# Kernel optimization log

Hardware: AMD Instinct MI355X
Metric: run time of the kernel (lower is better)

## Reference

```python
import jax, jax.numpy as jnp
import numpy as np

DIM = 1024; SD = 1024; N_BANDS = 4; MIMO_P = 8; BATCH = 2; L = 2048
LOG10000 = float(np.log(10000.0))


def _hippo_freqs(sd):
    n = jnp.arange(sd, dtype=jnp.float32)
    f = jnp.sqrt(2.0 * n + 1.0)
    f = f / f[-1]
    return jnp.exp(-f * LOG10000)


def setup_inputs() -> dict:
    key = jax.random.key(0)
    ks = jax.random.split(key, 16)
    dim, sd = DIM, SD
    wscale = 1.0 / np.sqrt(dim)
    n = jnp.arange(sd, dtype=jnp.float32)
    b0 = jnp.sqrt(2.0 * n + 1.0); b0 = b0 / b0[-1]
    b0_inv = jnp.log(jnp.expm1(jnp.clip(b0, 1e-6, None)))  # softplus^-1 of hippo b
    G = sd // MIMO_P
    inp = dict(
        x=jax.random.normal(ks[0], (BATCH, L, dim), jnp.float32),
        z_prev=jax.random.normal(ks[1], (BATCH, L, dim), jnp.float32),
        W_psi=jax.random.normal(ks[2], (2 * sd, dim), jnp.float32) * wscale,
        b_psi=jnp.zeros(2 * sd, jnp.float32),
        W_phi=jax.random.normal(ks[3], (2 * sd, dim), jnp.float32) * wscale,
        b_phi=jnp.zeros(2 * sd, jnp.float32),
        W_gate=jax.random.normal(ks[4], (1, dim), jnp.float32) * wscale,
        b_gate=jnp.zeros(1, jnp.float32),
        surprise_gain=jnp.zeros(1, jnp.float32),
        omega=_hippo_freqs(sd),
        log_gamma=jax.random.normal(ks[5], (sd,), jnp.float32) * 0.5 - 7.0,
        dt=jnp.float32(np.log(np.expm1(0.1))),  # layer_idx=0, depth=1 -> target_dt=0.1
        W_bs=jax.random.normal(ks[6], (sd, dim), jnp.float32) * 0.02,
        b_bs=b0_inv,
        W_ps=jax.random.uniform(ks[7], (sd, dim), jnp.float32, -wscale, wscale),
        b_ps=jnp.zeros(sd, jnp.float32),
        W_btx=jax.random.normal(ks[8], (sd, dim), jnp.float32) * 0.02,
        b_btx=b0_inv,
        W_bth=jax.random.normal(ks[9], (sd, 2 * sd), jnp.float32) * 0.02,
        b_bth=jnp.zeros(sd, jnp.float32),
        W_ptx=jax.random.uniform(ks[10], (sd, dim), jnp.float32, -wscale, wscale),
        b_ptx=jnp.zeros(sd, jnp.float32),
        mimo_w=jnp.eye(MIMO_P, dtype=jnp.float32)[None].repeat(G, 0)
               + 0.02 * jax.random.normal(ks[11], (G, MIMO_P, MIMO_P), jnp.float32),
        tau=jnp.ones(1, jnp.float32),
        beta=jnp.zeros(1, jnp.float32),
    )
    return inp


def _forward(x, z_prev, W_psi, b_psi, W_phi, b_phi, W_gate, b_gate, surprise_gain,
             omega, log_gamma, dt, W_bs, b_bs, W_ps, b_ps, W_btx, b_btx,
             W_bth, b_bth, W_ptx, b_ptx, mimo_w, tau, beta):
    Bsz, Ls, D = x.shape
    sd = omega.shape[0]
    n_fft = 1 << (2 * Ls - 1).bit_length()  # static

    # unitary mask: band 0 = lowest hippo frequencies (slowest modes) stay lossless
    freqs = _hippo_freqs(sd)
    order = jnp.argsort(freqs)
    band0 = order[: sd // N_BANDS]
    not_unitary = jnp.ones(sd, jnp.float32).at[band0].set(0.0)

    lin = lambda a, W, bb: a @ W.T + bb

    psi_raw = lin(x, W_psi, b_psi)
    psi = jax.lax.complex(psi_raw[..., :sd], psi_raw[..., sd:])
    phi_raw = lin(x, W_phi, b_phi)
    phi = jax.lax.complex(phi_raw[..., :sd], phi_raw[..., sd:])

    gate = jax.nn.sigmoid(lin(x, W_gate, b_gate))  # [B,L,1]
    surprise = jnp.mean(jnp.abs(x - z_prev), -1, keepdims=True)
    gate = gate * (1.0 + jnp.tanh(surprise_gain) * surprise)

    dt_eff = jax.nn.softplus(dt)
    gamma_eff = jax.nn.softplus(log_gamma) * not_unitary
    lam = jax.lax.complex(-gamma_eff, omega)  # [SD]
    t = jnp.arange(Ls, dtype=jnp.float32)
    kernel_raw = jnp.exp(lam[None, :] * (t[:, None] * dt_eff))  # [L,SD] A^t
    k_pad = jnp.concatenate([jnp.zeros((2, sd), kernel_raw.dtype), kernel_raw], 0)
    kernel_simpson = (k_pad[2:] + 4.0 * k_pad[1:-1] + k_pad[:-2]) / 6.0  # Simpson taps

    Kf_scout = jnp.fft.fft(kernel_raw.T, n=n_fft, axis=1)      # [SD,n_fft]
    Kf_true = jnp.fft.fft(kernel_simpson.T, n=n_fft, axis=1)

    def fftconv(U, Kf):  # causal conv via FFT: U [B,L,SD] complex
        Uf = jnp.fft.fft(jnp.transpose(U, (0, 2, 1)), n=n_fft, axis=2)
        H = jnp.fft.ifft(Uf * Kf[None], axis=2)[:, :, :Ls]
        return jnp.transpose(H, (0, 2, 1))

    # ---- scout wave: input-only LTI ----
    b_scout = jax.nn.softplus(lin(x, W_bs, b_bs))
    ph_s = jnp.pi * jnp.tanh(lin(x, W_ps, b_ps))
    Bc_s = jax.lax.complex(b_scout * jnp.cos(ph_s), b_scout * jnp.sin(ph_s))
    U_scout = gate * Bc_s * psi
    H_scout = fftconv(U_scout, Kf_scout)
    H_prev = jnp.pad(H_scout, ((0, 0), (1, 0), (0, 0)))[:, :-1]  # shift by 1
    scout_rms = jnp.sqrt(jnp.mean(H_prev.real ** 2 + H_prev.imag ** 2, -1, keepdims=True) + 1e-6)
    Hn = H_prev / scout_rms
    H_flat = jnp.concatenate([Hn.real, Hn.imag], -1)  # [B,L,2SD]

    # ---- true wave: state-dependent B, Simpson quadrature kernel ----
    b_true = jax.nn.softplus(lin(x, W_btx, b_btx) + lin(H_flat, W_bth, b_bth))
    ph_t = jnp.pi * jnp.tanh(lin(x, W_ptx, b_ptx))
    Bc_t = jax.lax.complex(b_true * jnp.cos(ph_t), b_true * jnp.sin(ph_t))
    U_true = gate * Bc_t * psi
    H = fftconv(U_true, Kf_true)

    read_rms = jnp.sqrt(jnp.mean(H.real ** 2 + H.imag ** 2, -1, keepdims=True) + 1e-6)
    Hn2 = H / read_rms

    # block-diagonal MIMO mixing in groups of mimo_p
    G = sd // MIMO_P
    Hg = Hn2.reshape(Bsz, Ls, G, MIMO_P)
    Hm = jnp.einsum('blgp,gpq->blgq', Hg, mimo_w.astype(Hg.dtype)).reshape(Bsz, Ls, sd)

    # Born-rule measurement: out = Re(h * phi^*), affine read temperature
    out = jnp.real(Hm * jnp.conj(phi))
    return tau * out + beta  # SD == dim -> out_proj is Identity


def reference(x, z_prev, W_psi, b_psi, W_phi, b_phi, W_gate, b_gate, surprise_gain,
              omega, log_gamma, dt, W_bs, b_bs, W_ps, b_ps, W_btx, b_btx,
              W_bth, b_bth, W_ptx, b_ptx, mimo_w, tau, beta):
    return _forward(x, z_prev, W_psi, b_psi, W_phi, b_phi, W_gate, b_gate,
                    surprise_gain, omega, log_gamma, dt, W_bs, b_bs, W_ps, b_ps,
                    W_btx, b_btx, W_bth, b_bth, W_ptx, b_ptx, mimo_w, tau, beta)
```

## Files before the change

kernel.cpp:

```cpp
#include <hip/hip_runtime.h>
#include <math.h>

#define DIMX   1024
#define SDN    1024
#define BATCHN 2
#define LSEQ   2048
#define BLROWS (BATCHN*LSEQ)
#define NCHUNK 64
#define LCHUNK (LSEQ/NCHUNK)
#define PI_F   3.14159265358979f

typedef unsigned short ushort_t;
typedef unsigned int uint_t;
typedef __bf16 bf16_t;
typedef bf16_t bf16x8 __attribute__((ext_vector_type(8)));
typedef float f32x4 __attribute__((ext_vector_type(4)));

__device__ __forceinline__ float softplusf_(float x) {
  return x > 20.0f ? x : log1pf(expf(x));
}

__device__ __forceinline__ ushort_t f2bf_rne(float f) {
  unsigned u = __float_as_uint(f);
  u = u + 0x7fffu + ((u >> 16) & 1u);
  return (ushort_t)(u >> 16);
}

__device__ __forceinline__ float bf2f(ushort_t u) {
  return __uint_as_float(((unsigned)u) << 16);
}

__device__ __forceinline__ uint_t pk2(float2 v) {
  return (uint_t)f2bf_rne(v.x) | ((uint_t)f2bf_rne(v.y) << 16);
}
__device__ __forceinline__ float2 upk2(uint_t u) {
  return make_float2(__uint_as_float(u << 16), __uint_as_float(u & 0xffff0000u));
}

__device__ __forceinline__ float2 cfma2(float2 a, float2 v, float2 u) {
  float re = fmaf(a.x, v.x, fmaf(-a.y, v.y, u.x));
  float im = fmaf(a.x, v.y, fmaf(a.y, v.x, u.y));
  return make_float2(re, im);
}

__device__ __forceinline__ void gload_lds16(const ushort_t* g, ushort_t* l) {
  __builtin_amdgcn_global_load_lds(
      (const __attribute__((address_space(1))) void*)g,
      (__attribute__((address_space(3))) void*)l, 16, 0, 0);
}

__global__ __launch_bounds__(256) void wcvt_kernel(
    const float* __restrict__ x,
    const float* __restrict__ Wpsi, const float* __restrict__ Wphi,
    const float* __restrict__ Wbs, const float* __restrict__ Wps,
    const float* __restrict__ Wbtx, const float* __restrict__ Wptx,
    const float* __restrict__ Wbth,
    const float* __restrict__ b_psi, const float* __restrict__ b_phi,
    const float* __restrict__ b_bs, const float* __restrict__ b_ps,
    const float* __restrict__ b_btx, const float* __restrict__ b_ptx,
    ushort_t* __restrict__ xb, ushort_t* __restrict__ wcat,
    ushort_t* __restrict__ wbthb, float* __restrict__ bcat) {
  int b = blockIdx.x;
  if (b >= 14336) {
    int n = (b - 14336) * 256 + threadIdx.x;
    float v;
    if (n < 2048) v = b_psi[n];
    else if (n < 4096) v = b_phi[n - 2048];
    else if (n < 5120) v = b_bs[n - 4096];
    else if (n < 6144) v = b_ps[n - 5120];
    else if (n < 7168) v = b_btx[n - 6144];
    else v = b_ptx[n - 7168];
    bcat[n] = v;
    return;
  }
  const float* src; ushort_t* dst; int off;
  if (b < 4096)       { src = x;    dst = xb;               off = b; }
  else if (b < 6144)  { src = Wpsi; dst = wcat;             off = b - 4096; }
  else if (b < 8192)  { src = Wphi; dst = wcat + 2097152u;  off = b - 6144; }
  else if (b < 9216)  { src = Wbs;  dst = wcat + 4194304u;  off = b - 8192; }
  else if (b < 10240) { src = Wps;  dst = wcat + 5242880u;  off = b - 9216; }
  else if (b < 11264) { src = Wbtx; dst = wcat + 6291456u;  off = b - 10240; }
  else if (b < 12288) { src = Wptx; dst = wcat + 7340032u;  off = b - 11264; }
  else                { src = Wbth; dst = wbthb;            off = b - 12288; }
  int i = (off * 256 + threadIdx.x) * 4;
  float4 v = *(const float4*)(src + i);
  ushort4 o;
  o.x = f2bf_rne(v.x); o.y = f2bf_rne(v.y);
  o.z = f2bf_rne(v.z); o.w = f2bf_rne(v.w);
  *(ushort4*)(dst + i) = o;
}

__global__ void coef_kernel(const float* __restrict__ omega,
                            const float* __restrict__ log_gamma,
                            const float* __restrict__ dt,
                            float2* __restrict__ a_out,
                            float2* __restrict__ A_out) {
  int s = blockIdx.x * blockDim.x + threadIdx.x;
  if (s >= SDN) return;
  double dtv = (double)dt[0];
  double dte = dtv > 20.0 ? dtv : log1p(exp(dtv));
  double gam = 0.0;
  if (s < SDN - SDN / 4) {
    double lg = (double)log_gamma[s];
    gam = lg > 20.0 ? lg : log1p(exp(lg));
  }
  double th = (double)omega[s] * dte;
  double r  = exp(-gam * dte);
  a_out[s] = make_float2((float)(r * cos(th)), (float)(r * sin(th)));
  double thl = th * (double)LCHUNK;
  double rl  = exp(-gam * dte * (double)LCHUNK);
  A_out[s] = make_float2((float)(rl * cos(thl)), (float)(rl * sin(thl)));
}

__global__ __launch_bounds__(256) void gate_kernel(
    const float* __restrict__ x, const float* __restrict__ z,
    const float* __restrict__ Wg, const float* __restrict__ bg,
    const float* __restrict__ sg, float* __restrict__ gate) {
  int m = blockIdx.x * 4 + (threadIdx.x >> 6);
  int lane = threadIdx.x & 63;
  const float* xp = x + (size_t)m * DIMX;
  const float* zp = z + (size_t)m * DIMX;
  float dot = 0.f, sur = 0.f;
  for (int i = lane; i < DIMX; i += 64) {
    float xv = xp[i];
    dot = fmaf(xv, Wg[i], dot);
    sur += fabsf(xv - zp[i]);
  }
#pragma unroll
  for (int o = 32; o > 0; o >>= 1) {
    dot += __shfl_down(dot, o, 64);
    sur += __shfl_down(sur, o, 64);
  }
  if (lane == 0) {
    float gs = 1.f / (1.f + expf(-(dot + bg[0])));
    gate[m] = gs * (1.f + tanhf(sg[0]) * (sur * (1.f / DIMX)));
  }
}

template<int MODE>
__global__ __launch_bounds__(256, 2) void gemm_bf16(
    const ushort_t* __restrict__ Xb, const ushort_t* __restrict__ Wb,
    const float* __restrict__ bias, ushort_t* __restrict__ Cb) {
  __shared__ ushort_t As[2][4096];
  __shared__ ushort_t Bs[2][4096];
  const int tid = threadIdx.x;
  const int w = tid >> 6, l = tid & 63;
  int bm, bn, ldx, ldw;
  const ushort_t *Xp, *Wp;
  if (MODE == 0) {
    int b = blockIdx.x;
    int xcd = b & 7, idx = b >> 3;
    int tx = ((xcd & 3) << 4) + (idx & 15);
    int ty = ((xcd >> 2) << 4) + (idx >> 4);
    bm = ty << 7; bn = tx << 7;
    ldx = 1024; ldw = 1024;
    Xp = Xb; Wp = Wb;
  } else {
    bm = blockIdx.y << 7; bn = blockIdx.x << 7;
    ldx = 2048; ldw = 2048;
    Xp = Xb + blockIdx.z * 1024;
    Wp = Wb + blockIdx.z * 1024;
  }
  const int wr = w >> 1, wc = w & 1;

  const int srow = tid >> 2;
  const int c8 = (((tid & 3) - (tid >> 3)) & 3) << 3;
  const ushort_t* ga0 = Xp + (size_t)(bm + srow) * ldx + c8;
  const ushort_t* ga1 = Xp + (size_t)(bm + 64 + srow) * ldx + c8;
  const ushort_t* gb0 = Wp + (size_t)(bn + srow) * ldw + c8;
  const ushort_t* gb1 = Wp + (size_t)(bn + 64 + srow) * ldw + c8;

  f32x4 acc[4][4] = {};
  const int nk = 32;

#define STAGE(buf, kt)                                   \
  do {                                                   \
    gload_lds16(ga0 + (kt), &As[buf][w * 512]);          \
    gload_lds16(ga1 + (kt), &As[buf][2048 + w * 512]);   \
    gload_lds16(gb0 + (kt), &Bs[buf][w * 512]);          \
    gload_lds16(gb1 + (kt), &Bs[buf][2048 + w * 512]);   \
  } while (0)

  STAGE(0, 0);
  __syncthreads();

  const int rl = l & 15, kh = l >> 4;
  const int chunkp = (kh + (rl >> 1)) & 3;
  for (int kt = 0; kt < nk; ++kt) {
    int cur = kt & 1;
    if (kt + 1 < nk) STAGE(cur ^ 1, (kt + 1) * 32);
    const uint4* Af = (const uint4*)As[cur];
    const uint4* Bf = (const uint4*)Bs[cur];
    bf16x8 a[4], b[4];
#pragma unroll
    for (int i = 0; i < 4; ++i)
      a[i] = __builtin_bit_cast(bf16x8, Af[(wr * 64 + i * 16 + rl) * 4 + chunkp]);
#pragma unroll
    for (int j = 0; j < 4; ++j)
      b[j] = __builtin_bit_cast(bf16x8, Bf[(wc * 64 + j * 16 + rl) * 4 + chunkp]);
#pragma unroll
    for (int i = 0; i < 4; ++i)
#pragma unroll
      for (int j = 0; j < 4; ++j)
        acc[i][j] = __builtin_amdgcn_mfma_f32_16x16x32_bf16(a[i], b[j], acc[i][j], 0, 0, 0);
    __syncthreads();
  }
#undef STAGE

#pragma unroll
  for (int i = 0; i < 4; ++i) {
    int mrow = bm + wr * 64 + i * 16 + (l >> 4) * 4;
#pragma unroll
    for (int j = 0; j < 4; ++j) {
      int ncol = bn + wc * 64 + j * 16 + (l & 15);
      if (MODE == 0) {
        float bv = bias[ncol];
#pragma unroll
        for (int r = 0; r < 4; ++r)
          Cb[(size_t)(mrow + r) * 8192 + ncol] = f2bf_rne(acc[i][j][r] + bv);
      } else {
        ushort_t* P = Cb + (size_t)blockIdx.z * (4096u * 1024u);
#pragma unroll
        for (int r = 0; r < 4; ++r)
          P[(size_t)(mrow + r) * 1024 + ncol] = f2bf_rne(acc[i][j][r]);
      }
    }
  }
}


__global__ __launch_bounds__(256) void u_scout(
    const float* __restrict__ gate, const ushort_t* __restrict__ proj,
    uint_t* __restrict__ U) {
  int idx = blockIdx.x * 256 + threadIdx.x;
  int m = idx >> 10, s = idx & (SDN - 1);
  const ushort_t* pr = proj + ((size_t)m << 13);
  float g  = gate[m];
  float bv = softplusf_(bf2f(pr[4096 + s]));
  float ph = PI_F * tanhf(bf2f(pr[5120 + s]));
  float sph, cph;
  sincosf(ph, &sph, &cph);
  float br = bv * cph, bi = bv * sph;
  float pre = bf2f(pr[s]), pim = bf2f(pr[1024 + s]);
  U[idx] = pk2(make_float2(g * (br * pre - bi * pim), g * (br * pim + bi * pre)));
}

__global__ __launch_bounds__(256) void u_true(
    const float* __restrict__ gate, const ushort_t* __restrict__ proj,
    const ushort_t* __restrict__ P0, const ushort_t* __restrict__ P1,
    const float* __restrict__ b_bth, uint_t* __restrict__ U) {
  int idx = blockIdx.x * 256 + threadIdx.x;
  int m = idx >> 10, s = idx & (SDN - 1);
  const ushort_t* pr = proj + ((size_t)m << 13);
  float g  = gate[m];
  float blv = bf2f(pr[6144 + s]) + bf2f(P0[idx]) + bf2f(P1[idx]) + b_bth[s];
  float bv = softplusf_(blv);
  float ph = PI_F * tanhf(bf2f(pr[7168 + s]));
  float sph, cph;
  sincosf(ph, &sph, &cph);
  float br = bv * cph, bi = bv * sph;
  float pre = bf2f(pr[s]), pim = bf2f(pr[1024 + s]);
  U[idx] = pk2(make_float2(g * (br * pre - bi * pim), g * (br * pim + bi * pre)));
}

__global__ __launch_bounds__(256) void scan_stage1(
    const uint_t* __restrict__ U, const float2* __restrict__ a,
    float2* __restrict__ carry) {
  int s = blockIdx.x * 256 + threadIdx.x;
  int c = blockIdx.y, b = blockIdx.z;
  float2 av = a[s];
  float2 V = make_float2(0.f, 0.f);
  const uint_t* Up = U + (size_t)(b * LSEQ + c * LCHUNK) * SDN + s;
#pragma unroll 4
  for (int t = 0; t < LCHUNK; ++t)
    V = cfma2(av, V, upk2(Up[(size_t)t * SDN]));
  carry[(size_t)(b * NCHUNK + c) * SDN + s] = V;
}

__global__ __launch_bounds__(256) void scan_stage2(
    const float2* __restrict__ carry, const float2* __restrict__ A,
    float2* __restrict__ prefix) {
  int s = blockIdx.x * 256 + threadIdx.x;
  int b = blockIdx.z;
  float2 Av = A[s];
  float2 P = make_float2(0.f, 0.f);
  for (int c = 0; c < NCHUNK; ++c) {
    size_t off = (size_t)(b * NCHUNK + c) * SDN + s;
    prefix[off] = P;
    P = cfma2(Av, P, carry[off]);
  }
}

__global__ __launch_bounds__(256) void scan_stage3(
    const uint_t* __restrict__ U, const float2* __restrict__ a,
    const float2* __restrict__ prefix, uint_t* __restrict__ Vout) {
  int s = blockIdx.x * 256 + threadIdx.x;
  int c = blockIdx.y, b = blockIdx.z;
  float2 av = a[s];
  float2 V = prefix[(size_t)(b * NCHUNK + c) * SDN + s];
  size_t base = (size_t)(b * LSEQ + c * LCHUNK) * SDN + s;
#pragma unroll 4
  for (int t = 0; t < LCHUNK; ++t) {
    V = cfma2(av, V, upk2(U[base + (size_t)t * SDN]));
    Vout[base + (size_t)t * SDN] = pk2(V);
  }
}

__global__ __launch_bounds__(256) void hflat_kernel(
    const uint_t* __restrict__ V, ushort_t* __restrict__ Hflat) {
  int m = blockIdx.x;
  int t = m & (LSEQ - 1);
  float2 v[4];
  float sum = 0.f;
#pragma unroll
  for (int i = 0; i < 4; ++i) {
    int s = threadIdx.x + i * 256;
    float2 vv = make_float2(0.f, 0.f);
    if (t > 0) vv = upk2(V[(size_t)(m - 1) * SDN + s]);
    v[i] = vv;
    sum += vv.x * vv.x + vv.y * vv.y;
  }
  __shared__ float red[256];
  red[threadIdx.x] = sum;
  __syncthreads();
  for (int o = 128; o > 0; o >>= 1) {
    if (threadIdx.x < o) red[threadIdx.x] += red[threadIdx.x + o];
    __syncthreads();
  }
  float inv = 1.0f / sqrtf(red[0] * (1.f / SDN) + 1e-6f);
  ushort_t* hr = Hflat + ((size_t)m << 11);
#pragma unroll
  for (int i = 0; i < 4; ++i) {
    int s = threadIdx.x + i * 256;
    hr[s] = f2bf_rne(v[i].x * inv);
    hr[SDN + s] = f2bf_rne(v[i].y * inv);
  }
}

__global__ __launch_bounds__(256) void final_kernel(
    const uint_t* __restrict__ V, const ushort_t* __restrict__ proj,
    const float* __restrict__ mimo, const float* __restrict__ tau,
    const float* __restrict__ beta, float* __restrict__ out) {
  int bid = blockIdx.x;
  int m = ((bid & 7) << 9) | (bid >> 3);
  int t = m & (LSEQ - 1);
  __shared__ float2 hl[SDN];
  __shared__ float red[256];
  float sum = 0.f;
#pragma unroll
  for (int i = 0; i < 4; ++i) {
    int s = threadIdx.x + i * 256;
    float2 v0 = upk2(V[(size_t)m * SDN + s]);
    float2 v1 = make_float2(0.f, 0.f), v2 = make_float2(0.f, 0.f);
    if (t >= 1) v1 = upk2(V[(size_t)(m - 1) * SDN + s]);
    if (t >= 2) v2 = upk2(V[(size_t)(m - 2) * SDN + s]);
    float2 h = make_float2((v0.x + 4.f * v1.x + v2.x) * (1.f / 6.f),
                           (v0.y + 4.f * v1.y + v2.y) * (1.f / 6.f));
    hl[s] = h;
    sum += h.x * h.x + h.y * h.y;
  }
  red[threadIdx.x] = sum;
  __syncthreads();
  for (int o = 128; o > 0; o >>= 1) {
    if (threadIdx.x < o) red[threadIdx.x] += red[threadIdx.x + o];
    __syncthreads();
  }
  float inv = 1.0f / sqrtf(red[0] * (1.f / SDN) + 1e-6f);
  float tv = tau[0], bv = beta[0];
  const ushort_t* pp = proj + ((size_t)m << 13) + 2048;
#pragma unroll
  for (int i = 0; i < 4; ++i) {
    int s = threadIdx.x + i * 256;
    int g = s >> 3, q = s & 7;
    const float* wp = mimo + (size_t)g * 64 + q;
    float hr = 0.f, hi = 0.f;
#pragma unroll
    for (int p = 0; p < 8; ++p) {
      float wv = wp[p * 8];
      float2 hp = hl[(g << 3) + p];
      hr = fmaf(hp.x, wv, hr);
      hi = fmaf(hp.y, wv, hi);
    }
    hr *= inv; hi *= inv;
    float o1 = hr * bf2f(pp[s]) + hi * bf2f(pp[SDN + s]);
    out[(size_t)m * SDN + s] = tv * o1 + bv;
  }
}

extern "C" void kernel_launch(void* const* d_in, const int* in_sizes, int n_in,
                              void* d_out, int out_size, void* d_ws, size_t ws_size,
                              hipStream_t stream) {
  const float* x      = (const float*)d_in[0];
  const float* z_prev = (const float*)d_in[1];
  const float* W_psi  = (const float*)d_in[2];
  const float* b_psi  = (const float*)d_in[3];
  const float* W_phi  = (const float*)d_in[4];
  const float* b_phi  = (const float*)d_in[5];
  const float* W_gate = (const float*)d_in[6];
  const float* b_gate = (const float*)d_in[7];
  const float* s_gain = (const float*)d_in[8];
  const float* omega  = (const float*)d_in[9];
  const float* log_g  = (const float*)d_in[10];
  const float* dt     = (const float*)d_in[11];
  const float* W_bs   = (const float*)d_in[12];
  const float* b_bs   = (const float*)d_in[13];
  const float* W_ps   = (const float*)d_in[14];
  const float* b_ps   = (const float*)d_in[15];
  const float* W_btx  = (const float*)d_in[16];
  const float* b_btx  = (const float*)d_in[17];
  const float* W_bth  = (const float*)d_in[18];
  const float* b_bth  = (const float*)d_in[19];
  const float* W_ptx  = (const float*)d_in[20];
  const float* b_ptx  = (const float*)d_in[21];
  const float* mimo_w = (const float*)d_in[22];
  const float* tau    = (const float*)d_in[23];
  const float* beta   = (const float*)d_in[24];
  float* out = (float*)d_out;

  float* ws = (float*)d_ws;
  const size_t M1 = 1 << 20;
  ushort_t* proj   = (ushort_t*)ws;
  uint_t*   U      = (uint_t*)(ws + 16 * M1);
  uint_t*   V      = U;
  ushort_t* xb     = (ushort_t*)(ws + 24 * M1);
  ushort_t* wcat   = (ushort_t*)(ws + 26 * M1);
  ushort_t* P0     = wcat;
  ushort_t* P1     = wcat + 4u * 1024u * 1024u;
  ushort_t* wbthb  = (ushort_t*)(ws + 30 * M1);
  ushort_t* hflatB = (ushort_t*)(ws + 31 * M1);
  float*    bcat   = ws + 35 * M1;
  float*    gate   = bcat + 8192;
  float2*   ac     = (float2*)(gate + 4096);
  float2*   Ac     = ac + 1024;
  float2*   carry  = Ac + 1024;
  float2*   prefix = carry + 131072;
  (void)ws_size; (void)in_sizes; (void)n_in; (void)out_size;

  dim3 blk(256);
  dim3 sgrid(SDN / 256, NCHUNK, BATCHN);

  coef_kernel<<<dim3(4), blk, 0, stream>>>(omega, log_g, dt, ac, Ac);
  gate_kernel<<<dim3(BLROWS / 4), blk, 0, stream>>>(x, z_prev, W_gate, b_gate, s_gain, gate);
  wcvt_kernel<<<dim3(14368), blk, 0, stream>>>(
      x, W_psi, W_phi, W_bs, W_ps, W_btx, W_ptx, W_bth,
      b_psi, b_phi, b_bs, b_ps, b_btx, b_ptx,
      xb, wcat, wbthb, bcat);

  gemm_bf16<0><<<dim3(2048), blk, 0, stream>>>(xb, wcat, bcat, proj);

  u_scout<<<dim3(BLROWS * SDN / 256), blk, 0, stream>>>(gate, proj, U);
  scan_stage1<<<sgrid, blk, 0, stream>>>(U, ac, carry);
  scan_stage2<<<dim3(SDN / 256, 1, BATCHN), blk, 0, stream>>>(carry, Ac, prefix);
  scan_stage3<<<sgrid, blk, 0, stream>>>(U, ac, prefix, V);

  hflat_kernel<<<dim3(BLROWS), blk, 0, stream>>>(V, hflatB);
  gemm_bf16<1><<<dim3(8, 32, 2), blk, 0, stream>>>(hflatB, wbthb, bcat, P0);

  u_true<<<dim3(BLROWS * SDN / 256), blk, 0, stream>>>(gate, proj, P0, P1, b_bth, U);
  scan_stage1<<<sgrid, blk, 0, stream>>>(U, ac, carry);
  scan_stage2<<<dim3(SDN / 256, 1, BATCHN), blk, 0, stream>>>(carry, Ac, prefix);
  scan_stage3<<<sgrid, blk, 0, stream>>>(U, ac, prefix, V);

  final_kernel<<<dim3(BLROWS), blk, 0, stream>>>(V, proj, mimo_w, tau, beta, out);
}
```

Baseline: 239.2 us.

## Fuse prep kernels, vectorize U builders with fast math, unroll scans more

Merges the coefficient, gate and weight-conversion kernels into one prep kernel, and computes the gate from the same x loads used for the bf16 conversion. The u_scout and u_true kernels now handle two elements per thread with packed 32-bit loads and stores. They also use fast intrinsics (__expf/__logf softplus, an exp-based tanh, __sincosf) in place of precise libm calls. Scan loops get deeper unrolling. The goal is to cut launch overhead and redundant reads of x, and to make the elementwise kernels cheaper, at the cost of some accuracy in the transcendental functions.

```diff
diff --git a/kernel.cpp b/kernel.cpp
--- a/kernel.cpp
+++ b/kernel.cpp
@@ -16,10 +16,6 @@
 typedef bf16_t bf16x8 __attribute__((ext_vector_type(8)));
 typedef float f32x4 __attribute__((ext_vector_type(4)));
 
-__device__ __forceinline__ float softplusf_(float x) {
-  return x > 20.0f ? x : log1pf(expf(x));
-}
-
 __device__ __forceinline__ ushort_t f2bf_rne(float f) {
   unsigned u = __float_as_uint(f);
   u = u + 0x7fffu + ((u >> 16) & 1u);
@@ -43,14 +39,23 @@
   return make_float2(re, im);
 }
 
+__device__ __forceinline__ float fast_softplus(float x) {
+  return x > 15.f ? x : __logf(1.f + __expf(x));
+}
+__device__ __forceinline__ float fast_tanh(float x) {
+  float xc = fminf(fmaxf(x, -9.f), 9.f);
+  float t = __expf(2.f * xc);
+  return (t - 1.f) * __builtin_amdgcn_rcpf(t + 1.f);
+}
+
 __device__ __forceinline__ void gload_lds16(const ushort_t* g, ushort_t* l) {
   __builtin_amdgcn_global_load_lds(
       (const __attribute__((address_space(1))) void*)g,
       (__attribute__((address_space(3))) void*)l, 16, 0, 0);
 }
 
-__global__ __launch_bounds__(256) void wcvt_kernel(
-    const float* __restrict__ x,
+__global__ __launch_bounds__(256) void prep_kernel(
+    const float* __restrict__ x, const float* __restrict__ z_prev,
     const float* __restrict__ Wpsi, const float* __restrict__ Wphi,
     const float* __restrict__ Wbs, const float* __restrict__ Wps,
     const float* __restrict__ Wbtx, const float* __restrict__ Wptx,
@@ -58,11 +63,64 @@
     const float* __restrict__ b_psi, const float* __restrict__ b_phi,
     const float* __restrict__ b_bs, const float* __restrict__ b_ps,
     const float* __restrict__ b_btx, const float* __restrict__ b_ptx,
+    const float* __restrict__ Wg, const float* __restrict__ bg,
+    const float* __restrict__ sg,
+    const float* __restrict__ omega, const float* __restrict__ log_gamma,
+    const float* __restrict__ dt,
     ushort_t* __restrict__ xb, ushort_t* __restrict__ wcat,
-    ushort_t* __restrict__ wbthb, float* __restrict__ bcat) {
+    ushort_t* __restrict__ wbthb, float* __restrict__ bcat,
+    float* __restrict__ gate, float2* __restrict__ a_out,
+    float2* __restrict__ A_out) {
   int b = blockIdx.x;
-  if (b >= 14336) {
-    int n = (b - 14336) * 256 + threadIdx.x;
+  int tid = threadIdx.x;
+  if (b < 4096) {
+    int i = tid * 4;
+    const float* xp = x + (size_t)b * DIMX;
+    const float* zp = z_prev + (size_t)b * DIMX;
+    float4 xv = *(const float4*)(xp + i);
+    float4 zv = *(const float4*)(zp + i);
+    float4 wv = *(const float4*)(Wg + i);
+    ushort4 o;
+    o.x = f2bf_rne(xv.x); o.y = f2bf_rne(xv.y);
+    o.z = f2bf_rne(xv.z); o.w = f2bf_rne(xv.w);
+    *(ushort4*)(xb + (size_t)b * DIMX + i) = o;
+    float dot = xv.x * wv.x + xv.y * wv.y + xv.z * wv.z + xv.w * wv.w;
+    float sur = fabsf(xv.x - zv.x) + fabsf(xv.y - zv.y) +
+                fabsf(xv.z - zv.z) + fabsf(xv.w - zv.w);
+    __shared__ float sdot[256], ssur[256];
+    sdot[tid] = dot; ssur[tid] = sur;
+    __syncthreads();
+    for (int o_ = 128; o_ > 0; o_ >>= 1) {
+      if (tid < o_) { sdot[tid] += sdot[tid + o_]; ssur[tid] += ssur[tid + o_]; }
+      __syncthreads();
+    }
+    if (tid == 0) {
+      float gs = 1.f / (1.f + expf(-(sdot[0] + bg[0])));
+      gate[b] = gs * (1.f + tanhf(sg[0]) * (ssur[0] * (1.f / DIMX)));
+    }
+    return;
+  }
+  b -= 4096;
+  if (b < 10240) {
+    const float* src; ushort_t* dst; int off;
+    if (b < 2048)       { src = Wpsi; dst = wcat;             off = b; }
+    else if (b < 4096)  { src = Wphi; dst = wcat + 2097152u;  off = b - 2048; }
+    else if (b < 5120)  { src = Wbs;  dst = wcat + 4194304u;  off = b - 4096; }
+    else if (b < 6144)  { src = Wps;  dst = wcat + 5242880u;  off = b - 5120; }
+    else if (b < 7168)  { src = Wbtx; dst = wcat + 6291456u;  off = b - 6144; }
+    else if (b < 8192)  { src = Wptx; dst = wcat + 7340032u;  off = b - 7168; }
+    else                { src = Wbth; dst = wbthb;            off = b - 8192; }
+    int i = (off * 256 + tid) * 4;
+    float4 v = *(const float4*)(src + i);
+    ushort4 o;
+    o.x = f2bf_rne(v.x); o.y = f2bf_rne(v.y);
+    o.z = f2bf_rne(v.z); o.w = f2bf_rne(v.w);
+    *(ushort4*)(dst + i) = o;
+    return;
+  }
+  b -= 10240;
+  if (b < 32) {
+    int n = b * 256 + tid;
     float v;
     if (n < 2048) v = b_psi[n];
     else if (n < 4096) v = b_phi[n - 2048];
@@ -73,30 +131,7 @@
     bcat[n] = v;
     return;
   }
-  const float* src; ushort_t* dst; int off;
-  if (b < 4096)       { src = x;    dst = xb;               off = b; }
-  else if (b < 6144)  { src = Wpsi; dst = wcat;             off = b - 4096; }
-  else if (b < 8192)  { src = Wphi; dst = wcat + 2097152u;  off = b - 6144; }
-  else if (b < 9216)  { src = Wbs;  dst = wcat + 4194304u;  off = b - 8192; }
-  else if (b < 10240) { src = Wps;  dst = wcat + 5242880u;  off = b - 9216; }
-  else if (b < 11264) { src = Wbtx; dst = wcat + 6291456u;  off = b - 10240; }
-  else if (b < 12288) { src = Wptx; dst = wcat + 7340032u;  off = b - 11264; }
-  else                { src = Wbth; dst = wbthb;            off = b - 12288; }
-  int i = (off * 256 + threadIdx.x) * 4;
-  float4 v = *(const float4*)(src + i);
-  ushort4 o;
-  o.x = f2bf_rne(v.x); o.y = f2bf_rne(v.y);
-  o.z = f2bf_rne(v.z); o.w = f2bf_rne(v.w);
-  *(ushort4*)(dst + i) = o;
-}
-
-__global__ void coef_kernel(const float* __restrict__ omega,
-                            const float* __restrict__ log_gamma,
-                            const float* __restrict__ dt,
-                            float2* __restrict__ a_out,
-                            float2* __restrict__ A_out) {
-  int s = blockIdx.x * blockDim.x + threadIdx.x;
-  if (s >= SDN) return;
+  int s = (b - 32) * 256 + tid;
   double dtv = (double)dt[0];
   double dte = dtv > 20.0 ? dtv : log1p(exp(dtv));
   double gam = 0.0;
@@ -110,31 +145,6 @@
   double thl = th * (double)LCHUNK;
   double rl  = exp(-gam * dte * (double)LCHUNK);
   A_out[s] = make_float2((float)(rl * cos(thl)), (float)(rl * sin(thl)));
-}
-
-__global__ __launch_bounds__(256) void gate_kernel(
-    const float* __restrict__ x, const float* __restrict__ z,
-    const float* __restrict__ Wg, const float* __restrict__ bg,
-    const float* __restrict__ sg, float* __restrict__ gate) {
-  int m = blockIdx.x * 4 + (threadIdx.x >> 6);
-  int lane = threadIdx.x & 63;
-  const float* xp = x + (size_t)m * DIMX;
-  const float* zp = z + (size_t)m * DIMX;
-  float dot = 0.f, sur = 0.f;
-  for (int i = lane; i < DIMX; i += 64) {
-    float xv = xp[i];
-    dot = fmaf(xv, Wg[i], dot);
-    sur += fabsf(xv - zp[i]);
-  }
-#pragma unroll
-  for (int o = 32; o > 0; o >>= 1) {
-    dot += __shfl_down(dot, o, 64);
-    sur += __shfl_down(sur, o, 64);
-  }
-  if (lane == 0) {
-    float gs = 1.f / (1.f + expf(-(dot + bg[0])));
-    gate[m] = gs * (1.f + tanhf(sg[0]) * (sur * (1.f / DIMX)));
-  }
 }
 
 template<int MODE>
@@ -232,35 +242,62 @@
 __global__ __launch_bounds__(256) void u_scout(
     const float* __restrict__ gate, const ushort_t* __restrict__ proj,
     uint_t* __restrict__ U) {
-  int idx = blockIdx.x * 256 + threadIdx.x;
-  int m = idx >> 10, s = idx & (SDN - 1);
+  int idx2 = blockIdx.x * 256 + threadIdx.x;
+  int m = idx2 >> 9, sp = (idx2 & 511) << 1;
   const ushort_t* pr = proj + ((size_t)m << 13);
-  float g  = gate[m];
-  float bv = softplusf_(bf2f(pr[4096 + s]));
-  float ph = PI_F * tanhf(bf2f(pr[5120 + s]));
-  float sph, cph;
-  sincosf(ph, &sph, &cph);
-  float br = bv * cph, bi = bv * sph;
-  float pre = bf2f(pr[s]), pim = bf2f(pr[1024 + s]);
-  U[idx] = pk2(make_float2(g * (br * pre - bi * pim), g * (br * pim + bi * pre)));
+  float g = gate[m];
+  uint_t bsu = *(const uint_t*)(pr + 4096 + sp);
+  uint_t psu = *(const uint_t*)(pr + 5120 + sp);
+  uint_t pre = *(const uint_t*)(pr + sp);
+  uint_t pim = *(const uint_t*)(pr + 1024 + sp);
+  uint_t o[2];
+#pragma unroll
+  for (int e = 0; e < 2; ++e) {
+    float bv = fast_softplus(bf2f((ushort_t)(e ? (bsu >> 16) : (bsu & 0xffff))));
+    float ph = PI_F * fast_tanh(bf2f((ushort_t)(e ? (psu >> 16) : (psu & 0xffff))));
+    float sph, cph;
+    __sincosf(ph, &sph, &cph);
+    float br = bv * cph, bi = bv * sph;
+    float prf = bf2f((ushort_t)(e ? (pre >> 16) : (pre & 0xffff)));
+    float pif = bf2f((ushort_t)(e ? (pim >> 16) : (pim & 0xffff)));
+    o[e] = pk2(make_float2(g * (br * prf - bi * pif), g * (br * pif + bi * prf)));
+  }
+  *(uint2*)(U + ((size_t)m << 10) + sp) = make_uint2(o[0], o[1]);
 }
 
 __global__ __launch_bounds__(256) void u_true(
     const float* __restrict__ gate, const ushort_t* __restrict__ proj,
     const ushort_t* __restrict__ P0, const ushort_t* __restrict__ P1,
     const float* __restrict__ b_bth, uint_t* __restrict__ U) {
-  int idx = blockIdx.x * 256 + threadIdx.x;
-  int m = idx >> 10, s = idx & (SDN - 1);
+  int idx2 = blockIdx.x * 256 + threadIdx.x;
+  int m = idx2 >> 9, sp = (idx2 & 511) << 1;
   const ushort_t* pr = proj + ((size_t)m << 13);
-  float g  = gate[m];
-  float blv = bf2f(pr[6144 + s]) + bf2f(P0[idx]) + bf2f(P1[idx]) + b_bth[s];
-  float bv = softplusf_(blv);
-  float ph = PI_F * tanhf(bf2f(pr[7168 + s]));
-  float sph, cph;
-  sincosf(ph, &sph, &cph);
-  float br = bv * cph, bi = bv * sph;
-  float pre = bf2f(pr[s]), pim = bf2f(pr[1024 + s]);
-  U[idx] = pk2(make_float2(g * (br * pre - bi * pim), g * (br * pim + bi * pre)));
+  float g = gate[m];
+  size_t base = ((size_t)m << 10) + sp;
+  uint_t btu = *(const uint_t*)(pr + 6144 + sp);
+  uint_t ptu = *(const uint_t*)(pr + 7168 + sp);
+  uint_t p0u = *(const uint_t*)(P0 + base);
+  uint_t p1u = *(const uint_t*)(P1 + base);
+  float2 bb = *(const float2*)(b_bth + sp);
+  uint_t pre = *(const uint_t*)(pr + sp);
+  uint_t pim = *(const uint_t*)(pr + 1024 + sp);
+  uint_t o[2];
+#pragma unroll
+  for (int e = 0; e < 2; ++e) {
+    float blv = bf2f((ushort_t)(e ? (btu >> 16) : (btu & 0xffff)))
+              + bf2f((ushort_t)(e ? (p0u >> 16) : (p0u & 0xffff)))
+              + bf2f((ushort_t)(e ? (p1u >> 16) : (p1u & 0xffff)))
+              + (e ? bb.y : bb.x);
+    float bv = fast_softplus(blv);
+    float ph = PI_F * fast_tanh(bf2f((ushort_t)(e ? (ptu >> 16) : (ptu & 0xffff))));
+    float sph, cph;
+    __sincosf(ph, &sph, &cph);
+    float br = bv * cph, bi = bv * sph;
+    float prf = bf2f((ushort_t)(e ? (pre >> 16) : (pre & 0xffff)));
+    float pif = bf2f((ushort_t)(e ? (pim >> 16) : (pim & 0xffff)));
+    o[e] = pk2(make_float2(g * (br * prf - bi * pif), g * (br * pif + bi * prf)));
+  }
+  *(uint2*)(U + base) = make_uint2(o[0], o[1]);
 }
 
 __global__ __launch_bounds__(256) void scan_stage1(
@@ -271,7 +308,7 @@
   float2 av = a[s];
   float2 V = make_float2(0.f, 0.f);
   const uint_t* Up = U + (size_t)(b * LSEQ + c * LCHUNK) * SDN + s;
-#pragma unroll 4
+#pragma unroll 8
   for (int t = 0; t < LCHUNK; ++t)
     V = cfma2(av, V, upk2(Up[(size_t)t * SDN]));
   carry[(size_t)(b * NCHUNK + c) * SDN + s] = V;
@@ -284,6 +321,7 @@
   int b = blockIdx.z;
   float2 Av = A[s];
   float2 P = make_float2(0.f, 0.f);
+#pragma unroll 8
   for (int c = 0; c < NCHUNK; ++c) {
     size_t off = (size_t)(b * NCHUNK + c) * SDN + s;
     prefix[off] = P;
@@ -299,7 +337,7 @@
   float2 av = a[s];
   float2 V = prefix[(size_t)(b * NCHUNK + c) * SDN + s];
   size_t base = (size_t)(b * LSEQ + c * LCHUNK) * SDN + s;
-#pragma unroll 4
+#pragma unroll 8
   for (int t = 0; t < LCHUNK; ++t) {
     V = cfma2(av, V, upk2(U[base + (size_t)t * SDN]));
     Vout[base + (size_t)t * SDN] = pk2(V);
@@ -439,16 +477,15 @@
   dim3 blk(256);
   dim3 sgrid(SDN / 256, NCHUNK, BATCHN);
 
-  coef_kernel<<<dim3(4), blk, 0, stream>>>(omega, log_g, dt, ac, Ac);
-  gate_kernel<<<dim3(BLROWS / 4), blk, 0, stream>>>(x, z_prev, W_gate, b_gate, s_gain, gate);
-  wcvt_kernel<<<dim3(14368), blk, 0, stream>>>(
-      x, W_psi, W_phi, W_bs, W_ps, W_btx, W_ptx, W_bth,
+  prep_kernel<<<dim3(14372), blk, 0, stream>>>(
+      x, z_prev, W_psi, W_phi, W_bs, W_ps, W_btx, W_ptx, W_bth,
       b_psi, b_phi, b_bs, b_ps, b_btx, b_ptx,
-      xb, wcat, wbthb, bcat);
+      W_gate, b_gate, s_gain, omega, log_g, dt,
+      xb, wcat, wbthb, bcat, gate, ac, Ac);
 
   gemm_bf16<0><<<dim3(2048), blk, 0, stream>>>(xb, wcat, bcat, proj);
 
-  u_scout<<<dim3(BLROWS * SDN / 256), blk, 0, stream>>>(gate, proj, U);
+  u_scout<<<dim3(BLROWS * SDN / 512), blk, 0, stream>>>(gate, proj, U);
   scan_stage1<<<sgrid, blk, 0, stream>>>(U, ac, carry);
   scan_stage2<<<dim3(SDN / 256, 1, BATCHN), blk, 0, stream>>>(carry, Ac, prefix);
   scan_stage3<<<sgrid, blk, 0, stream>>>(U, ac, prefix, V);
@@ -456,7 +493,7 @@
   hflat_kernel<<<dim3(BLROWS), blk, 0, stream>>>(V, hflatB);
   gemm_bf16<1><<<dim3(8, 32, 2), blk, 0, stream>>>(hflatB, wbthb, bcat, P0);
 
-  u_true<<<dim3(BLROWS * SDN / 256), blk, 0, stream>>>(gate, proj, P0, P1, b_bth, U);
+  u_true<<<dim3(BLROWS * SDN / 512), blk, 0, stream>>>(gate, proj, P0, P1, b_bth, U);
   scan_stage1<<<sgrid, blk, 0, stream>>>(U, ac, carry);
   scan_stage2<<<dim3(SDN / 256, 1, BATCHN), blk, 0, stream>>>(carry, Ac, prefix);
   scan_stage3<<<sgrid, blk, 0, stream>>>(U, ac, prefix, V);
```

Result: faster. 209.4 us (-12.5%).
